# Kernel optimization log

Hardware: AMD Instinct MI355X
Metric: run time of the kernel (lower is better)

The kernel has to match this reference:

```python
import jax, jax.numpy as jnp
import numpy as np

B, N, C, H = 4, 1024, 512, 8
HD = C // H
SCALE = HD ** -0.5
LN_EPS = 1e-5


def setup_inputs() -> dict:
    key = jax.random.key(0)
    ks = jax.random.split(key, 4)
    return {
        "x": jax.random.normal(ks[0], (B, N, C), dtype=jnp.float32),
        "Wqkv": jax.random.normal(ks[1], (C, 3 * C), dtype=jnp.float32) * (C ** -0.5),
        "bqkv": jnp.zeros((3 * C,), dtype=jnp.float32),
        "order_weights": jnp.ones((3,), dtype=jnp.float32),
        "Wproj": jax.random.normal(ks[2], (C, C), dtype=jnp.float32) * (C ** -0.5),
        "bproj": jnp.zeros((C,), dtype=jnp.float32),
        "gamma": jnp.ones((C,), dtype=jnp.float32),
        "beta": jnp.zeros((C,), dtype=jnp.float32),
    }


def reference(x, Wqkv, bqkv, order_weights, Wproj, bproj, gamma, beta):
    b, n, c = x.shape
    qkv = (x @ Wqkv + bqkv).reshape(b, n, 3, H, HD)
    qkv = jnp.transpose(qkv, (2, 0, 3, 1, 4))  # [3, B, H, N, HD]
    q, k, v = qkv[0], qkv[1], qkv[2]

    base = jnp.einsum('bhnd,bhmd->bhnm', q, k) * SCALE  # [B, H, N, N]

    ow = jax.nn.softmax(order_weights)
    # torch loop: term_0 = base, term_i = base**(i+1)
    attn = ow[0] * base
    cur = base
    for i in range(1, order_weights.shape[0]):
        cur = cur * base
        attn = attn + ow[i] * cur

    attn_final = jax.nn.softmax(attn, axis=-1)

    out = jnp.einsum('bhnm,bhmd->bhnd', attn_final, v)
    out = jnp.transpose(out, (0, 2, 1, 3)).reshape(b, n, c)
    out = out @ Wproj + bproj

    y = x + out
    mu = jnp.mean(y, axis=-1, keepdims=True)
    var = jnp.var(y, axis=-1, keepdims=True)
    y = (y - mu) / jnp.sqrt(var + LN_EPS) * gamma + beta
    return y, attn_final
```

## Files before the change

kernel.cpp:

```cpp
#include <hip/hip_runtime.h>
#include <math.h>

#define B_ 4
#define N_ 1024
#define C_ 512
#define H_ 8
#define HD_ 64
#define SCALE_ 0.125f
#define LN_EPS_ 1e-5f

typedef _Float16 f16x8 __attribute__((ext_vector_type(8)));
typedef float f32x4 __attribute__((ext_vector_type(4)));

__device__ __forceinline__ void cvt_split(const float4& A, const float4& Bv,
                                          f16x8& hi, f16x8& lo) {
    float v[8] = {A.x, A.y, A.z, A.w, Bv.x, Bv.y, Bv.z, Bv.w};
#pragma unroll
    for (int i = 0; i < 8; ++i) {
        _Float16 h = (_Float16)v[i];
        hi[i] = h;
        lo[i] = (_Float16)(v[i] - (float)h);
    }
}

__global__ __launch_bounds__(256) void wsplit_qkv(const float* __restrict__ W,
                                                  _Float16* __restrict__ wt_hi,
                                                  _Float16* __restrict__ wt_lo) {
    __shared__ float tile[64][65];
    const int tid = threadIdx.x;
    const int n0 = blockIdx.x * 64;
    const int k0 = blockIdx.y * 64;
#pragma unroll
    for (int i = 0; i < 16; ++i) {
        int e = tid + i * 256;
        int kk = e >> 6, nn = e & 63;
        tile[kk][nn] = W[(size_t)(k0 + kk) * (3 * C_) + n0 + nn];
    }
    __syncthreads();
#pragma unroll
    for (int i = 0; i < 16; ++i) {
        int e = tid + i * 256;
        int n = e >> 6, k = e & 63;
        float v = tile[k][n];
        _Float16 h = (_Float16)v;
        wt_hi[(size_t)(n0 + n) * C_ + k0 + k] = h;
        wt_lo[(size_t)(n0 + n) * C_ + k0 + k] = (_Float16)(v - (float)h);
    }
}

__global__ __launch_bounds__(256) void qkv_gemm_mfma(const float* __restrict__ x,
                                                     const _Float16* __restrict__ wt_hi,
                                                     const _Float16* __restrict__ wt_lo,
                                                     const float* __restrict__ bqkv,
                                                     float* __restrict__ qkv) {
    const int tid = threadIdx.x;
    const int lane = tid & 63;
    const int w = tid >> 6;
    const int r16 = lane & 15;
    const int g = lane >> 4;
    const int row0 = blockIdx.x * 32;
    const int col0 = blockIdx.y * 256 + w * 64;

    f32x4 acc[2][4] = {};

    const float* xr0 = x + (size_t)(row0 + r16) * C_;
    const float* xr1 = x + (size_t)(row0 + 16 + r16) * C_;

    for (int kt = 0; kt < 16; ++kt) {
        const int k0 = kt * 32 + 8 * g;
        f16x8 aHi0, aLo0, aHi1, aLo1;
        {
            float4 a0 = *(const float4*)&xr0[k0];
            float4 a1 = *(const float4*)&xr0[k0 + 4];
            cvt_split(a0, a1, aHi0, aLo0);
            float4 b0 = *(const float4*)&xr1[k0];
            float4 b1 = *(const float4*)&xr1[k0 + 4];
            cvt_split(b0, b1, aHi1, aLo1);
        }
#pragma unroll
        for (int ct = 0; ct < 4; ++ct) {
            const int c = col0 + ct * 16 + r16;
            f16x8 bHi = *(const f16x8*)&wt_hi[(size_t)c * C_ + k0];
            f16x8 bLo = *(const f16x8*)&wt_lo[(size_t)c * C_ + k0];
            acc[0][ct] = __builtin_amdgcn_mfma_f32_16x16x32_f16(aHi0, bHi, acc[0][ct], 0, 0, 0);
            acc[0][ct] = __builtin_amdgcn_mfma_f32_16x16x32_f16(aHi0, bLo, acc[0][ct], 0, 0, 0);
            acc[0][ct] = __builtin_amdgcn_mfma_f32_16x16x32_f16(aLo0, bHi, acc[0][ct], 0, 0, 0);
            acc[1][ct] = __builtin_amdgcn_mfma_f32_16x16x32_f16(aHi1, bHi, acc[1][ct], 0, 0, 0);
            acc[1][ct] = __builtin_amdgcn_mfma_f32_16x16x32_f16(aHi1, bLo, acc[1][ct], 0, 0, 0);
            acc[1][ct] = __builtin_amdgcn_mfma_f32_16x16x32_f16(aLo1, bHi, acc[1][ct], 0, 0, 0);
        }
    }

#pragma unroll
    for (int rt = 0; rt < 2; ++rt)
#pragma unroll
        for (int ct = 0; ct < 4; ++ct) {
            const int c = col0 + ct * 16 + r16;
            const float bias = bqkv[c];
#pragma unroll
            for (int j = 0; j < 4; ++j) {
                const int r = row0 + rt * 16 + 4 * g + j;
                qkv[(size_t)r * (3 * C_) + c] = acc[rt][ct][j] + bias;
            }
        }
}

__global__ __launch_bounds__(256) void attn_scores(const float* __restrict__ qkv,
                                                   const float* __restrict__ ow_in,
                                                   float* __restrict__ attn) {
    __shared__ float smax[4][16];
    __shared__ float ssum[4][16];

    const int tid = threadIdx.x;
    const int lane = tid & 63;
    const int w = tid >> 6;
    const int r16 = lane & 15;
    const int g = lane >> 4;
    const int n0 = blockIdx.x * 16;
    const int bh = blockIdx.y;
    const int b = bh >> 3, h = bh & 7;
    const size_t RS = 3 * C_;

    float w0 = ow_in[0], w1 = ow_in[1], w2 = ow_in[2];
    float wm = fmaxf(w0, fmaxf(w1, w2));
    float e0 = __expf(w0 - wm), e1 = __expf(w1 - wm), e2 = __expf(w2 - wm);
    float einv = 1.0f / (e0 + e1 + e2);
    float ow0 = e0 * einv, ow1 = e1 * einv, ow2 = e2 * einv;

    const float* qrow = qkv + (size_t)(b * N_ + n0 + r16) * RS + h * HD_;
    f16x8 aHi0, aLo0, aHi1, aLo1;
    {
        float4 qa = ((const float4*)qrow)[2 * g + 0];
        float4 qb = ((const float4*)qrow)[2 * g + 1];
        float4 qc = ((const float4*)qrow)[8 + 2 * g];
        float4 qd = ((const float4*)qrow)[9 + 2 * g];
        cvt_split(qa, qb, aHi0, aLo0);
        cvt_split(qc, qd, aHi1, aLo1);
    }

    float p[16][4];

    const float* kbase = qkv + (size_t)(b * N_) * RS + C_ + h * HD_;
#pragma unroll
    for (int t = 0; t < 16; ++t) {
        const int ct = w * 16 + t;
        const float* krow = kbase + (size_t)(ct * 16 + r16) * RS;
        float4 ka = ((const float4*)krow)[2 * g + 0];
        float4 kb = ((const float4*)krow)[2 * g + 1];
        float4 kc = ((const float4*)krow)[8 + 2 * g];
        float4 kd = ((const float4*)krow)[9 + 2 * g];
        f16x8 bHi0, bLo0, bHi1, bLo1;
        cvt_split(ka, kb, bHi0, bLo0);
        cvt_split(kc, kd, bHi1, bLo1);

        f32x4 acc = {0.f, 0.f, 0.f, 0.f};
        acc = __builtin_amdgcn_mfma_f32_16x16x32_f16(aHi0, bHi0, acc, 0, 0, 0);
        acc = __builtin_amdgcn_mfma_f32_16x16x32_f16(aHi0, bLo0, acc, 0, 0, 0);
        acc = __builtin_amdgcn_mfma_f32_16x16x32_f16(aLo0, bHi0, acc, 0, 0, 0);
        acc = __builtin_amdgcn_mfma_f32_16x16x32_f16(aHi1, bHi1, acc, 0, 0, 0);
        acc = __builtin_amdgcn_mfma_f32_16x16x32_f16(aHi1, bLo1, acc, 0, 0, 0);
        acc = __builtin_amdgcn_mfma_f32_16x16x32_f16(aLo1, bHi1, acc, 0, 0, 0);

#pragma unroll
        for (int j = 0; j < 4; ++j) {
            float s = acc[j] * SCALE_;
            p[t][j] = s * (ow0 + s * (ow1 + s * ow2));
        }
    }

    float rmax[4] = {-1e30f, -1e30f, -1e30f, -1e30f};
#pragma unroll
    for (int t = 0; t < 16; ++t)
#pragma unroll
        for (int j = 0; j < 4; ++j) rmax[j] = fmaxf(rmax[j], p[t][j]);
#pragma unroll
    for (int j = 0; j < 4; ++j)
#pragma unroll
        for (int m = 1; m < 16; m <<= 1)
            rmax[j] = fmaxf(rmax[j], __shfl_xor(rmax[j], m, 64));
    if (r16 == 0) {
#pragma unroll
        for (int j = 0; j < 4; ++j) smax[w][g * 4 + j] = rmax[j];
    }
    __syncthreads();
    float gm[4];
#pragma unroll
    for (int j = 0; j < 4; ++j) {
        int rr = g * 4 + j;
        gm[j] = fmaxf(fmaxf(smax[0][rr], smax[1][rr]),
                      fmaxf(smax[2][rr], smax[3][rr]));
    }

    float rsum[4] = {0.f, 0.f, 0.f, 0.f};
#pragma unroll
    for (int t = 0; t < 16; ++t)
#pragma unroll
        for (int j = 0; j < 4; ++j) {
            float e = __expf(p[t][j] - gm[j]);
            p[t][j] = e;
            rsum[j] += e;
        }
#pragma unroll
    for (int j = 0; j < 4; ++j)
#pragma unroll
        for (int m = 1; m < 16; m <<= 1)
            rsum[j] += __shfl_xor(rsum[j], m, 64);
    if (r16 == 0) {
#pragma unroll
        for (int j = 0; j < 4; ++j) ssum[w][g * 4 + j] = rsum[j];
    }
    __syncthreads();
    float inv[4];
#pragma unroll
    for (int j = 0; j < 4; ++j) {
        int rr = g * 4 + j;
        inv[j] = 1.0f / (ssum[0][rr] + ssum[1][rr] + ssum[2][rr] + ssum[3][rr]);
    }

    float* abase = attn + ((size_t)bh * N_ + n0 + 4 * g) * N_ + w * 256 + r16;
#pragma unroll
    for (int j = 0; j < 4; ++j) {
        float* arow = abase + (size_t)j * N_;
        float sc = inv[j];
#pragma unroll
        for (int t = 0; t < 16; ++t)
            arow[t * 16] = p[t][j] * sc;
    }
}

__global__ __launch_bounds__(256) void pv_gemm(const float* __restrict__ qkv,
                                               const float* __restrict__ attn,
                                               float* __restrict__ ctx) {
    __shared__ __align__(16) float Pst[64][68];
    __shared__ __align__(16) float Vs[64][68];

    const int tid = threadIdx.x;
    const int tx = tid & 15;
    const int ty = tid >> 4;
    const int n0 = blockIdx.x * 64;
    const int bh = blockIdx.y;
    const int b = bh >> 3, h = bh & 7;
    const size_t RS = 3 * C_;

    const int rr = tid >> 2;
    const int q = tid & 3;

    float acc[4][4] = {};

    for (int mt = 0; mt < 16; ++mt) {
        const int m0 = mt * 64;
        const float* prow = attn + ((size_t)bh * N_ + n0 + rr) * N_ + m0 + q * 16;
        const float* vrow = qkv + (size_t)(b * N_ + m0 + rr) * RS + 2 * C_ + h * HD_ + q * 16;
        float4 pv[4], vv[4];
#pragma unroll
        for (int m = 0; m < 4; ++m) pv[m] = ((const float4*)prow)[m];
#pragma unroll
        for (int m = 0; m < 4; ++m) vv[m] = ((const float4*)vrow)[m];
        __syncthreads();
#pragma unroll
        for (int m = 0; m < 4; ++m) {
            int c = q * 16 + m * 4;
            Pst[c + 0][rr] = pv[m].x; Pst[c + 1][rr] = pv[m].y;
            Pst[c + 2][rr] = pv[m].z; Pst[c + 3][rr] = pv[m].w;
            *(float4*)&Vs[rr][c] = vv[m];
        }
        __syncthreads();
#pragma unroll 16
        for (int mm = 0; mm < 64; ++mm) {
            float4 a4 = *(const float4*)&Pst[mm][ty * 4];
            float4 b4 = *(const float4*)&Vs[mm][tx * 4];
            float a[4] = {a4.x, a4.y, a4.z, a4.w};
            float bb[4] = {b4.x, b4.y, b4.z, b4.w};
#pragma unroll
            for (int i = 0; i < 4; ++i)
#pragma unroll
                for (int j = 0; j < 4; ++j) acc[i][j] += a[i] * bb[j];
        }
    }
#pragma unroll
    for (int i = 0; i < 4; ++i) {
        float4 o;
        o.x = acc[i][0]; o.y = acc[i][1]; o.z = acc[i][2]; o.w = acc[i][3];
        *(float4*)&ctx[(size_t)(b * N_ + n0 + ty * 4 + i) * C_ + h * HD_ + tx * 4] = o;
    }
}

__global__ __launch_bounds__(256) void proj_gemm(const float* __restrict__ ctx,
                                                 const float* __restrict__ x,
                                                 const float* __restrict__ Wproj,
                                                 const float* __restrict__ bproj,
                                                 float* __restrict__ y) {
    const int K = C_;
    const int NN = C_;
    __shared__ float As[64][17];
    __shared__ float Bs[16][64];

    const int tid = threadIdx.x;
    const int tx = tid & 15;
    const int ty = tid >> 4;
    const int row0 = blockIdx.y * 64;
    const int col0 = blockIdx.x * 64;

    float acc[4][4] = {};

    for (int kt = 0; kt < K; kt += 16) {
        {
            int lin = tid * 4;
            int m = lin >> 4;
            int k = lin & 15;
            float4 a = *(const float4*)&ctx[(size_t)(row0 + m) * K + kt + k];
            As[m][k + 0] = a.x; As[m][k + 1] = a.y;
            As[m][k + 2] = a.z; As[m][k + 3] = a.w;
        }
        {
            int lin = tid * 4;
            int kk = lin >> 6;
            int n = lin & 63;
            *(float4*)&Bs[kk][n] =
                *(const float4*)&Wproj[(size_t)(kt + kk) * NN + col0 + n];
        }
        __syncthreads();
#pragma unroll
        for (int kk = 0; kk < 16; ++kk) {
            float a[4], bb[4];
#pragma unroll
            for (int i = 0; i < 4; ++i) a[i] = As[ty * 4 + i][kk];
#pragma unroll
            for (int j = 0; j < 4; ++j) bb[j] = Bs[kk][tx * 4 + j];
#pragma unroll
            for (int i = 0; i < 4; ++i)
#pragma unroll
                for (int j = 0; j < 4; ++j) acc[i][j] += a[i] * bb[j];
        }
        __syncthreads();
    }
#pragma unroll
    for (int i = 0; i < 4; ++i) {
        int r = row0 + ty * 4 + i;
        int c = col0 + tx * 4;
        float4 xr = *(const float4*)&x[(size_t)r * C_ + c];
        float4 o;
        o.x = acc[i][0] + bproj[c + 0] + xr.x;
        o.y = acc[i][1] + bproj[c + 1] + xr.y;
        o.z = acc[i][2] + bproj[c + 2] + xr.z;
        o.w = acc[i][3] + bproj[c + 3] + xr.w;
        *(float4*)&y[(size_t)r * C_ + c] = o;
    }
}

__global__ __launch_bounds__(256) void ln_kernel(float* __restrict__ y,
                                                 const float* __restrict__ gamma,
                                                 const float* __restrict__ beta) {
    __shared__ float wsum[4], wsq[4];
    const int row = blockIdx.x;
    const int tid = threadIdx.x;
    const int lane = tid & 63;
    const int w = tid >> 6;

    float2 v = ((const float2*)(y + (size_t)row * C_))[tid];
    float s = v.x + v.y;
    float sq = v.x * v.x + v.y * v.y;
#pragma unroll
    for (int m = 1; m < 64; m <<= 1) {
        s += __shfl_xor(s, m, 64);
        sq += __shfl_xor(sq, m, 64);
    }
    if (lane == 0) { wsum[w] = s; wsq[w] = sq; }
    __syncthreads();
    float ts = wsum[0] + wsum[1] + wsum[2] + wsum[3];
    float tq = wsq[0] + wsq[1] + wsq[2] + wsq[3];
    float mu = ts * (1.0f / C_);
    float var = tq * (1.0f / C_) - mu * mu;
    float rstd = rsqrtf(var + LN_EPS_);

    float2 g = ((const float2*)gamma)[tid];
    float2 be = ((const float2*)beta)[tid];
    float2 o;
    o.x = (v.x - mu) * rstd * g.x + be.x;
    o.y = (v.y - mu) * rstd * g.y + be.y;
    ((float2*)(y + (size_t)row * C_))[tid] = o;
}

extern "C" void kernel_launch(void* const* d_in, const int* in_sizes, int n_in,
                              void* d_out, int out_size, void* d_ws, size_t ws_size,
                              hipStream_t stream) {
    const float* x     = (const float*)d_in[0];
    const float* Wqkv  = (const float*)d_in[1];
    const float* bqkv  = (const float*)d_in[2];
    const float* ow    = (const float*)d_in[3];
    const float* Wproj = (const float*)d_in[4];
    const float* bproj = (const float*)d_in[5];
    const float* gamma = (const float*)d_in[6];
    const float* beta  = (const float*)d_in[7];

    float* out  = (float*)d_out;
    float* y    = out;
    float* attn = out + (size_t)B_ * N_ * C_;
    float* qkv  = (float*)d_ws;
    float* ctx  = qkv + (size_t)B_ * N_ * 3 * C_;

    _Float16* wt_hi = (_Float16*)attn;
    _Float16* wt_lo = wt_hi + (size_t)(3 * C_) * C_;

    dim3 g0(3 * C_ / 64, C_ / 64);
    wsplit_qkv<<<g0, 256, 0, stream>>>(Wqkv, wt_hi, wt_lo);

    dim3 g1(B_ * N_ / 32, 3 * C_ / 256);
    qkv_gemm_mfma<<<g1, 256, 0, stream>>>(x, wt_hi, wt_lo, bqkv, qkv);

    dim3 g2(N_ / 16, B_ * H_);
    attn_scores<<<g2, 256, 0, stream>>>(qkv, ow, attn);

    dim3 g3(N_ / 64, B_ * H_);
    pv_gemm<<<g3, 256, 0, stream>>>(qkv, attn, ctx);

    dim3 g4(C_ / 64, B_ * N_ / 64);
    proj_gemm<<<g4, 256, 0, stream>>>(ctx, x, Wproj, bproj, y);

    ln_kernel<<<B_ * N_, 256, 0, stream>>>(y, gamma, beta);
}
```

Before: 417.4 us.

## Use split-fp16 MFMA for attention-times-V with pre-transposed V

Replaces the scalar FP32 LDS-tiled P·V GEMM with MFMA 16x16x32 f16 instructions. Precision is kept by splitting values into hi/lo fp16 parts and summing three products. A new kernel transposes V into hi/lo fp16 buffers laid out d-major, stored in the output y region before y is written. P is read straight from global memory per lane without LDS staging. This adds a launch and extra V traffic, and the fp16 split may lose some accuracy compared with FP32.

Result: no change. 422.5 us (+1.2%).

```diff
diff --git a/kernel.cpp b/kernel.cpp
--- a/kernel.cpp
+++ b/kernel.cpp
@@ -45,6 +45,34 @@
         _Float16 h = (_Float16)v;
         wt_hi[(size_t)(n0 + n) * C_ + k0 + k] = h;
         wt_lo[(size_t)(n0 + n) * C_ + k0 + k] = (_Float16)(v - (float)h);
+    }
+}
+
+__global__ __launch_bounds__(256) void vsplit_v(const float* __restrict__ qkv,
+                                                _Float16* __restrict__ vt_hi,
+                                                _Float16* __restrict__ vt_lo) {
+    __shared__ float tile[64][65];
+    const int tid = threadIdx.x;
+    const int m0 = blockIdx.x * 64;
+    const int bh = blockIdx.y;
+    const int b = bh >> 3, h = bh & 7;
+    const size_t RS = 3 * C_;
+#pragma unroll
+    for (int i = 0; i < 16; ++i) {
+        int e = tid + i * 256;
+        int mm = e >> 6, d = e & 63;
+        tile[mm][d] = qkv[(size_t)(b * N_ + m0 + mm) * RS + 2 * C_ + h * HD_ + d];
+    }
+    __syncthreads();
+#pragma unroll
+    for (int i = 0; i < 16; ++i) {
+        int e = tid + i * 256;
+        int d = e >> 6, mm = e & 63;
+        float v = tile[mm][d];
+        _Float16 hh = (_Float16)v;
+        size_t idx = ((size_t)bh * HD_ + d) * N_ + m0 + mm;
+        vt_hi[idx] = hh;
+        vt_lo[idx] = (_Float16)(v - (float)hh);
     }
 }
 
@@ -228,60 +256,50 @@
     }
 }
 
-__global__ __launch_bounds__(256) void pv_gemm(const float* __restrict__ qkv,
-                                               const float* __restrict__ attn,
+__global__ __launch_bounds__(256) void pv_mfma(const float* __restrict__ attn,
+                                               const _Float16* __restrict__ vt_hi,
+                                               const _Float16* __restrict__ vt_lo,
                                                float* __restrict__ ctx) {
-    __shared__ __align__(16) float Pst[64][68];
-    __shared__ __align__(16) float Vs[64][68];
-
-    const int tid = threadIdx.x;
-    const int tx = tid & 15;
-    const int ty = tid >> 4;
+    const int tid = threadIdx.x;
+    const int lane = tid & 63;
+    const int w = tid >> 6;
+    const int r16 = lane & 15;
+    const int g = lane >> 4;
     const int n0 = blockIdx.x * 64;
     const int bh = blockIdx.y;
     const int b = bh >> 3, h = bh & 7;
-    const size_t RS = 3 * C_;
-
-    const int rr = tid >> 2;
-    const int q = tid & 3;
-
-    float acc[4][4] = {};
-
-    for (int mt = 0; mt < 16; ++mt) {
-        const int m0 = mt * 64;
-        const float* prow = attn + ((size_t)bh * N_ + n0 + rr) * N_ + m0 + q * 16;
-        const float* vrow = qkv + (size_t)(b * N_ + m0 + rr) * RS + 2 * C_ + h * HD_ + q * 16;
-        float4 pv[4], vv[4];
-#pragma unroll
-        for (int m = 0; m < 4; ++m) pv[m] = ((const float4*)prow)[m];
-#pragma unroll
-        for (int m = 0; m < 4; ++m) vv[m] = ((const float4*)vrow)[m];
-        __syncthreads();
-#pragma unroll
-        for (int m = 0; m < 4; ++m) {
-            int c = q * 16 + m * 4;
-            Pst[c + 0][rr] = pv[m].x; Pst[c + 1][rr] = pv[m].y;
-            Pst[c + 2][rr] = pv[m].z; Pst[c + 3][rr] = pv[m].w;
-            *(float4*)&Vs[rr][c] = vv[m];
-        }
-        __syncthreads();
-#pragma unroll 16
-        for (int mm = 0; mm < 64; ++mm) {
-            float4 a4 = *(const float4*)&Pst[mm][ty * 4];
-            float4 b4 = *(const float4*)&Vs[mm][tx * 4];
-            float a[4] = {a4.x, a4.y, a4.z, a4.w};
-            float bb[4] = {b4.x, b4.y, b4.z, b4.w};
-#pragma unroll
-            for (int i = 0; i < 4; ++i)
-#pragma unroll
-                for (int j = 0; j < 4; ++j) acc[i][j] += a[i] * bb[j];
-        }
-    }
-#pragma unroll
-    for (int i = 0; i < 4; ++i) {
-        float4 o;
-        o.x = acc[i][0]; o.y = acc[i][1]; o.z = acc[i][2]; o.w = acc[i][3];
-        *(float4*)&ctx[(size_t)(b * N_ + n0 + ty * 4 + i) * C_ + h * HD_ + tx * 4] = o;
+
+    const float* prow = attn + ((size_t)bh * N_ + n0 + w * 16 + r16) * N_;
+    const _Float16* vh = vt_hi + (size_t)bh * HD_ * N_;
+    const _Float16* vl = vt_lo + (size_t)bh * HD_ * N_;
+
+    f32x4 acc[4] = {};
+
+    for (int kt = 0; kt < 32; ++kt) {
+        const int k0 = kt * 32 + 8 * g;
+        float4 a0 = *(const float4*)&prow[k0];
+        float4 a1 = *(const float4*)&prow[k0 + 4];
+        f16x8 aHi, aLo;
+        cvt_split(a0, a1, aHi, aLo);
+#pragma unroll
+        for (int ct = 0; ct < 4; ++ct) {
+            const int d = ct * 16 + r16;
+            f16x8 bHi = *(const f16x8*)&vh[(size_t)d * N_ + k0];
+            f16x8 bLo = *(const f16x8*)&vl[(size_t)d * N_ + k0];
+            acc[ct] = __builtin_amdgcn_mfma_f32_16x16x32_f16(aHi, bHi, acc[ct], 0, 0, 0);
+            acc[ct] = __builtin_amdgcn_mfma_f32_16x16x32_f16(aHi, bLo, acc[ct], 0, 0, 0);
+            acc[ct] = __builtin_amdgcn_mfma_f32_16x16x32_f16(aLo, bHi, acc[ct], 0, 0, 0);
+        }
+    }
+
+#pragma unroll
+    for (int ct = 0; ct < 4; ++ct) {
+        const int c = h * HD_ + ct * 16 + r16;
+#pragma unroll
+        for (int j = 0; j < 4; ++j) {
+            const int r = n0 + w * 16 + 4 * g + j;
+            ctx[(size_t)(b * N_ + r) * C_ + c] = acc[ct][j];
+        }
     }
 }
 
@@ -401,6 +419,8 @@
 
     _Float16* wt_hi = (_Float16*)attn;
     _Float16* wt_lo = wt_hi + (size_t)(3 * C_) * C_;
+    _Float16* vt_hi = (_Float16*)y;
+    _Float16* vt_lo = vt_hi + (size_t)B_ * H_ * HD_ * N_;
 
     dim3 g0(3 * C_ / 64, C_ / 64);
     wsplit_qkv<<<g0, 256, 0, stream>>>(Wqkv, wt_hi, wt_lo);
@@ -408,11 +428,14 @@
     dim3 g1(B_ * N_ / 32, 3 * C_ / 256);
     qkv_gemm_mfma<<<g1, 256, 0, stream>>>(x, wt_hi, wt_lo, bqkv, qkv);
 
+    dim3 gv(N_ / 64, B_ * H_);
+    vsplit_v<<<gv, 256, 0, stream>>>(qkv, vt_hi, vt_lo);
+
     dim3 g2(N_ / 16, B_ * H_);
     attn_scores<<<g2, 256, 0, stream>>>(qkv, ow, attn);
 
     dim3 g3(N_ / 64, B_ * H_);
-    pv_gemm<<<g3, 256, 0, stream>>>(qkv, attn, ctx);
+    pv_mfma<<<g3, 256, 0, stream>>>(attn, vt_hi, vt_lo, ctx);
 
     dim3 g4(C_ / 64, B_ * N_ / 64);
     proj_gemm<<<g4, 256, 0, stream>>>(ctx, x, Wproj, bproj, y);
```
